# Optimization experiments

Measured on AMD Instinct MI355X. Metric: run time of the kernel, lower is better.

Reference implementation:

```python
import jax, jax.numpy as jnp
import numpy as np

B, S, D = 2, 2048, 1024
H, HD = 16, 64  # num_heads, head_dim; D == H*HD


def setup_inputs() -> dict:
    key = jax.random.key(0)
    k_x, k_wa, k_wp = jax.random.split(key, 3)
    x = jax.random.normal(k_x, (B, S, D), dtype=jnp.float32)
    w_attn = jax.random.normal(k_wa, (D, 3 * D), dtype=jnp.float32) * (1.0 / np.sqrt(D))
    b_attn = jnp.zeros((3 * D,), dtype=jnp.float32)
    w_proj = jax.random.normal(k_wp, (D, D), dtype=jnp.float32) * (1.0 / np.sqrt(D))
    b_proj = jnp.zeros((D,), dtype=jnp.float32)
    return {"x": x, "w_attn": w_attn, "b_attn": b_attn, "w_proj": w_proj, "b_proj": b_proj}


def reference(x, w_attn, b_attn, w_proj, b_proj):
    # c_attn: [B,S,D] -> [B,S,3D], split into q,k,v
    qkv = jnp.einsum('bsd,df->bsf', x, w_attn) + b_attn
    q, k, v = jnp.split(qkv, 3, axis=-1)
    # split heads: [B,S,D] -> [B,S,H,HD]
    q = q.reshape(B, S, H, HD)
    k = k.reshape(B, S, H, HD)
    v = v.reshape(B, S, H, HD)
    scale = 1.0 / jnp.sqrt(jnp.float32(HD))
    # scores: [B,H,S,S]
    scores = jnp.einsum('bnhd,bmhd->bhnm', q, k) * scale
    causal_mask = jnp.tril(jnp.ones((S, S), dtype=jnp.bool_))
    scores = jnp.where(causal_mask, scores, jnp.float32(-1e9))
    attn = jax.nn.softmax(scores, axis=-1)
    # dropout is identity (inference=True / p=0)
    out = jnp.einsum('bhnm,bmhd->bnhd', attn, v)
    out = out.reshape(B, S, D)
    out = jnp.einsum('bsd,de->bse', out, w_proj) + b_proj
    return out
```

## Files before the change

kernel.cpp:

```cpp
#include <hip/hip_runtime.h>

#define Bn 2
#define Sn 2048
#define Dn 1024
#define Hn 16
#define HDn 64

typedef unsigned short u16;
typedef u16 u16x4 __attribute__((ext_vector_type(4)));
typedef u16 u16x8 __attribute__((ext_vector_type(8)));
typedef __bf16 bf16x8 __attribute__((ext_vector_type(8)));
typedef float f32x4 __attribute__((ext_vector_type(4)));

__device__ __forceinline__ u16 cvt1(float f) {
  __bf16 h = (__bf16)f;
  return __builtin_bit_cast(u16, h);
}

__device__ __forceinline__ f32x4 mfma16(u16x8 a, u16x8 b, f32x4 c) {
  return __builtin_amdgcn_mfma_f32_16x16x32_bf16(
      __builtin_bit_cast(bf16x8, a), __builtin_bit_cast(bf16x8, b), c, 0, 0, 0);
}

__device__ __forceinline__ int xorv(int row) {
  return (row & 7) ^ ((row >> 3) & 7);
}
__device__ __forceinline__ int swzb(int row, int bytecol) {
  return row * 128 + (bytecol ^ (xorv(row) << 4));
}

__global__ __launch_bounds__(256) void k_cvt(const float* __restrict__ in,
                                             u16* __restrict__ out, int n4) {
  int i = blockIdx.x * 256 + threadIdx.x;
  if (i < n4) {
    const float4 v = reinterpret_cast<const float4*>(in)[i];
    u16x4 o = {cvt1(v.x), cvt1(v.y), cvt1(v.z), cvt1(v.w)};
    reinterpret_cast<u16x4*>(out)[i] = o;
  }
}

__global__ __launch_bounds__(256) void k_transpose(const float* __restrict__ in,
                                                   u16* __restrict__ out,
                                                   int K, int N) {
  __shared__ u16 tile[32][33];
  const int n0 = blockIdx.x * 32, k0 = blockIdx.y * 32;
  const int tx = threadIdx.x, ty = threadIdx.y;
#pragma unroll
  for (int r = 0; r < 4; ++r) {
    const int k = ty * 4 + r;
    tile[k][tx] = cvt1(in[(size_t)(k0 + k) * N + n0 + tx]);
  }
  __syncthreads();
#pragma unroll
  for (int r = 0; r < 4; ++r) {
    const int n = ty * 4 + r;
    out[(size_t)(n0 + n) * K + k0 + tx] = tile[tx][n];
  }
}

__global__ __launch_bounds__(512) void k_gemm2(
    const u16* __restrict__ A, const u16* __restrict__ Bt, int K,
    const float* __restrict__ bias, u16* __restrict__ oq, u16* __restrict__ ok,
    u16* __restrict__ ov, float* __restrict__ of, int mode) {
  __shared__ __align__(16) u16 a_lds[2][8192];
  __shared__ __align__(16) u16 b_lds[2][8192];
  const int tid = threadIdx.x;
  const int lane = tid & 63, w = tid >> 6;
  const int wr = w >> 2, wc = w & 3;
  const int lm = lane & 15, lk = lane >> 4;
  const int m0 = blockIdx.y * 128, n0 = blockIdx.x * 128;
  const int NT = K >> 6;

  const int srow0 = tid >> 3;
  const int scb = (tid & 7) * 16;

  f32x4 acc[4][2] = {};

#define STAGE2(d, kt)                                                         \
  {                                                                           \
    _Pragma("unroll") for (int p = 0; p < 2; ++p) {                           \
      const int row = p * 64 + srow0;                                         \
      const int col = (scb ^ (xorv(row) << 4)) >> 1;                          \
      __builtin_amdgcn_global_load_lds(                                       \
          (const __attribute__((address_space(1))) void*)(A + (size_t)(m0 + row) * K + (kt) * 64 + col), \
          (__attribute__((address_space(3))) void*)(a_lds[d] + p * 4096 + tid * 8), \
          16, 0, 0);                                                          \
      __builtin_amdgcn_global_load_lds(                                       \
          (const __attribute__((address_space(1))) void*)(Bt + (size_t)(n0 + row) * K + (kt) * 64 + col), \
          (__attribute__((address_space(3))) void*)(b_lds[d] + p * 4096 + tid * 8), \
          16, 0, 0);                                                          \
    }                                                                         \
  }

  STAGE2(0, 0);
  __syncthreads();

  for (int t = 0; t < NT; ++t) {
    const int cur = t & 1;
    if (t + 1 < NT) STAGE2(cur ^ 1, t + 1);
    u16x8 av[4][2], bv[2][2];
#pragma unroll
    for (int m = 0; m < 4; ++m)
#pragma unroll
      for (int kk = 0; kk < 2; ++kk)
        av[m][kk] = *reinterpret_cast<const u16x8*>(
            (char*)a_lds[cur] + swzb(wr * 64 + m * 16 + lm, kk * 64 + lk * 16));
#pragma unroll
    for (int n = 0; n < 2; ++n)
#pragma unroll
      for (int kk = 0; kk < 2; ++kk)
        bv[n][kk] = *reinterpret_cast<const u16x8*>(
            (char*)b_lds[cur] + swzb(wc * 32 + n * 16 + lm, kk * 64 + lk * 16));
    __builtin_amdgcn_s_setprio(1);
#pragma unroll
    for (int kk = 0; kk < 2; ++kk)
#pragma unroll
      for (int m = 0; m < 4; ++m)
#pragma unroll
        for (int n = 0; n < 2; ++n)
          acc[m][n] = mfma16(av[m][kk], bv[n][kk], acc[m][n]);
    __builtin_amdgcn_s_setprio(0);
    __syncthreads();
  }
#undef STAGE2

#pragma unroll
  for (int m = 0; m < 4; ++m) {
#pragma unroll
    for (int n = 0; n < 2; ++n) {
      const int col = n0 + wc * 32 + n * 16 + lm;
      const float bb = bias[col];
      const int row0 = m0 + wr * 64 + m * 16 + lk * 4;
      if (mode == 0) {
        const int which = col >> 10;
        const int h = (col >> 6) & 15, hd = col & 63;
        const int b = row0 >> 11, s0 = row0 & 2047;
        if (which == 2) {
          u16x4 pk;
#pragma unroll
          for (int j = 0; j < 4; ++j) pk[j] = cvt1(acc[m][n][j] + bb);
          *reinterpret_cast<u16x4*>(
              ov + ((size_t)(b * Hn + h) * HDn + hd) * Sn + s0) = pk;
        } else {
          u16* dst = which == 0 ? oq : ok;
          const float sc = which == 0 ? 0.125f : 1.0f;
#pragma unroll
          for (int j = 0; j < 4; ++j)
            dst[((size_t)(b * Hn + h) * Sn + s0 + j) * HDn + hd] =
                cvt1((acc[m][n][j] + bb) * sc);
        }
      } else {
#pragma unroll
        for (int j = 0; j < 4; ++j)
          of[(size_t)(row0 + j) * Dn + col] = acc[m][n][j] + bb;
      }
    }
  }
}

__global__ __launch_bounds__(256) void k_attn(const u16* __restrict__ qb,
                                              const u16* __restrict__ kb,
                                              const u16* __restrict__ vtb,
                                              u16* __restrict__ ob) {
  const int bx = blockIdx.x;
  const int qt = 31 - (bx >> 5);
  const int bh = bx & 31;
  const int h = bh & 15, b = bh >> 4;
  const int tid = threadIdx.x, lane = tid & 63, w = tid >> 6;
  const int lm = lane & 15, lk = lane >> 4;
  const int Q0 = qt * 64;
  const int q0 = Q0 + w * 16;
  const size_t head = (size_t)(b * Hn + h) * Sn * HDn;
  const u16* Q = qb + head;
  const u16* Kp = kb + head;
  const u16* Vt = vtb + head;

  __shared__ __align__(16) u16 k_lds[64 * 64];
  __shared__ __align__(16) u16 vt_lds[64 * 64];
  __shared__ __align__(16) u16 p_lds[4][16 * 64];
  char* myp = (char*)p_lds[w];

  const int sr = tid >> 2, scb = (tid & 3) * 16;
  const u16* Ksrc = Kp + (size_t)sr * HDn + scb;
  const u16* Vsrc = Vt + (size_t)sr * Sn + scb;

  u16x8 aq[2];
#pragma unroll
  for (int c = 0; c < 2; ++c)
    aq[c] = *reinterpret_cast<const u16x8*>(Q + (size_t)(q0 + lm) * HDn + c * 32 + lk * 8);

  f32x4 o_acc[4] = {};
  float mrow = -1e30f, lrow = 0.f;
  const float C = 1.44269504f;

  const int nk = Q0 + 64;
  u16x8 kreg[2], vreg[2];
  kreg[0] = *reinterpret_cast<const u16x8*>(Ksrc);
  kreg[1] = *reinterpret_cast<const u16x8*>(Ksrc + 8);
  vreg[0] = *reinterpret_cast<const u16x8*>(Vsrc);
  vreg[1] = *reinterpret_cast<const u16x8*>(Vsrc + 8);

  for (int j0 = 0; j0 < nk; j0 += 64) {
    *reinterpret_cast<u16x8*>((char*)k_lds + swzb(sr, scb * 2)) = kreg[0];
    *reinterpret_cast<u16x8*>((char*)k_lds + swzb(sr, scb * 2 + 16)) = kreg[1];
    *reinterpret_cast<u16x8*>((char*)vt_lds + swzb(sr, scb * 2)) = vreg[0];
    *reinterpret_cast<u16x8*>((char*)vt_lds + swzb(sr, scb * 2 + 16)) = vreg[1];
    __syncthreads();
    if (j0 + 64 < nk) {
      const u16* kn = Ksrc + (size_t)(j0 + 64) * HDn;
      const u16* vn = Vsrc + (j0 + 64);
      kreg[0] = *reinterpret_cast<const u16x8*>(kn);
      kreg[1] = *reinterpret_cast<const u16x8*>(kn + 8);
      vreg[0] = *reinterpret_cast<const u16x8*>(vn);
      vreg[1] = *reinterpret_cast<const u16x8*>(vn + 8);
    }

    f32x4 s[4];
    __builtin_amdgcn_s_setprio(1);
#pragma unroll
    for (int kc = 0; kc < 4; ++kc) {
      const u16x8 kf0 = *reinterpret_cast<const u16x8*>((char*)k_lds + swzb(kc * 16 + lm, lk * 16));
      const u16x8 kf1 = *reinterpret_cast<const u16x8*>((char*)k_lds + swzb(kc * 16 + lm, 64 + lk * 16));
      f32x4 z = {};
      z = mfma16(kf0, aq[0], z);
      s[kc] = mfma16(kf1, aq[1], z);
    }
    __builtin_amdgcn_s_setprio(0);
    if (j0 + 63 > q0) {
#pragma unroll
      for (int kc = 0; kc < 4; ++kc)
#pragma unroll
        for (int jj = 0; jj < 4; ++jj)
          if (j0 + kc * 16 + lk * 4 + jj > q0 + lm) s[kc][jj] = -1e30f;
    }

    float vmax = -1e30f;
#pragma unroll
    for (int kc = 0; kc < 4; ++kc)
#pragma unroll
      for (int jj = 0; jj < 4; ++jj) vmax = fmaxf(vmax, s[kc][jj]);
    vmax = fmaxf(vmax, __shfl_xor(vmax, 16, 64));
    vmax = fmaxf(vmax, __shfl_xor(vmax, 32, 64));
    if (!__all(vmax - mrow <= 8.0f)) {
      const float mnew = fmaxf(mrow, vmax);
      const float alpha = exp2f((mrow - mnew) * C);
      mrow = mnew;
      lrow *= alpha;
      float a4[4];
#pragma unroll
      for (int jj = 0; jj < 4; ++jj) a4[jj] = __shfl(alpha, lk * 4 + jj, 64);
#pragma unroll
      for (int t = 0; t < 4; ++t)
#pragma unroll
        for (int jj = 0; jj < 4; ++jj) o_acc[t][jj] *= a4[jj];
    }
    const float mc = mrow * C;
    float psum = 0.f;
#pragma unroll
    for (int kc = 0; kc < 4; ++kc) {
      u16x4 pk;
#pragma unroll
      for (int jj = 0; jj < 4; ++jj) {
        const float p = exp2f(s[kc][jj] * C - mc);
        psum += p;
        pk[jj] = cvt1(p);
      }
      *reinterpret_cast<u16x4*>(myp + swzb(lm, kc * 32 + lk * 8)) = pk;
    }
    psum += __shfl_xor(psum, 16, 64);
    psum += __shfl_xor(psum, 32, 64);
    lrow += psum;

    __builtin_amdgcn_s_setprio(1);
#pragma unroll
    for (int kt = 0; kt < 2; ++kt) {
      const u16x8 pa = *reinterpret_cast<const u16x8*>(myp + swzb(lm, kt * 64 + lk * 16));
#pragma unroll
      for (int t = 0; t < 4; ++t) {
        const u16x8 vf = *reinterpret_cast<const u16x8*>((char*)vt_lds + swzb(t * 16 + lm, kt * 64 + lk * 16));
        o_acc[t] = mfma16(pa, vf, o_acc[t]);
      }
    }
    __builtin_amdgcn_s_setprio(0);
    __syncthreads();
  }

  float l4[4];
#pragma unroll
  for (int jj = 0; jj < 4; ++jj) l4[jj] = __shfl(lrow, lk * 4 + jj, 64);
#pragma unroll
  for (int t = 0; t < 4; ++t) {
#pragma unroll
    for (int jj = 0; jj < 4; ++jj) {
      const int rowg = q0 + lk * 4 + jj;
      const float val = o_acc[t][jj] / l4[jj];
      ob[((size_t)(b * Sn + rowg)) * Dn + h * HDn + t * 16 + lm] = cvt1(val);
    }
  }
}

extern "C" void kernel_launch(void* const* d_in, const int* in_sizes, int n_in,
                              void* d_out, int out_size, void* d_ws, size_t ws_size,
                              hipStream_t stream) {
  const float* x = (const float*)d_in[0];
  const float* w_attn = (const float*)d_in[1];
  const float* b_attn = (const float*)d_in[2];
  const float* w_proj = (const float*)d_in[3];
  const float* b_proj = (const float*)d_in[4];
  float* out = (float*)d_out;

  u16* ws = (u16*)d_ws;
  u16* xb = ws;
  u16* wat = xb + (size_t)4096 * 1024;
  u16* wpt = wat + (size_t)3072 * 1024;
  u16* qb = wpt + (size_t)1024 * 1024;
  u16* kb = qb + (size_t)Bn * Hn * Sn * HDn;
  u16* vtb = kb + (size_t)Bn * Hn * Sn * HDn;
  u16* ao = vtb + (size_t)Bn * Hn * Sn * HDn;

  k_cvt<<<4096, 256, 0, stream>>>(x, xb, 1048576);
  k_transpose<<<dim3(3072 / 32, 1024 / 32), dim3(32, 8), 0, stream>>>(w_attn, wat, 1024, 3072);
  k_transpose<<<dim3(1024 / 32, 1024 / 32), dim3(32, 8), 0, stream>>>(w_proj, wpt, 1024, 1024);
  k_gemm2<<<dim3(3072 / 128, 4096 / 128), 512, 0, stream>>>(xb, wat, 1024, b_attn, qb, kb, vtb, nullptr, 0);
  k_attn<<<Bn * Hn * (Sn / 64), 256, 0, stream>>>(qb, kb, vtb, ao);
  k_gemm2<<<dim3(1024 / 128, 4096 / 128), 512, 0, stream>>>(ao, wpt, 1024, b_proj, nullptr, nullptr, nullptr, out, 1);
}
```

Baseline: 188.7 us.

## Double attention query tile per block with double-buffered K/V and XCD-aware GEMM block remap

The attention kernel now processes 128 query rows per block (32 per wave, two 16-row fragments), so each K/V tile loaded into LDS is reused across twice as many queries. K/V LDS staging is double-buffered, which lets the next tile be written while the current one is consumed. Fully masked fragments skip their MFMAs. The GEMM remaps linear block IDs across 8 groups, intended to improve L2 locality per XCD. In exchange, the attention grid has half as many blocks and needs more registers, which can lower occupancy.

```diff
diff --git a/kernel.cpp b/kernel.cpp
--- a/kernel.cpp
+++ b/kernel.cpp
@@ -68,7 +68,11 @@
   const int lane = tid & 63, w = tid >> 6;
   const int wr = w >> 2, wc = w & 3;
   const int lm = lane & 15, lk = lane >> 4;
-  const int m0 = blockIdx.y * 128, n0 = blockIdx.x * 128;
+  const int nx = gridDim.x;
+  int lin = blockIdx.y * nx + blockIdx.x;
+  const int cpx = (nx * gridDim.y) >> 3;
+  lin = (lin & 7) * cpx + (lin >> 3);
+  const int m0 = (lin / nx) * 128, n0 = (lin % nx) * 128;
   const int NT = K >> 6;
 
   const int srow0 = tid >> 3;
@@ -163,138 +167,182 @@
                                               const u16* __restrict__ vtb,
                                               u16* __restrict__ ob) {
   const int bx = blockIdx.x;
-  const int qt = 31 - (bx >> 5);
+  const int qt = 15 - (bx >> 5);
   const int bh = bx & 31;
   const int h = bh & 15, b = bh >> 4;
   const int tid = threadIdx.x, lane = tid & 63, w = tid >> 6;
   const int lm = lane & 15, lk = lane >> 4;
-  const int Q0 = qt * 64;
-  const int q0 = Q0 + w * 16;
+  const int Q0 = qt * 128;
+  const int q0 = Q0 + w * 32;
   const size_t head = (size_t)(b * Hn + h) * Sn * HDn;
   const u16* Q = qb + head;
   const u16* Kp = kb + head;
   const u16* Vt = vtb + head;
 
-  __shared__ __align__(16) u16 k_lds[64 * 64];
-  __shared__ __align__(16) u16 vt_lds[64 * 64];
-  __shared__ __align__(16) u16 p_lds[4][16 * 64];
+  __shared__ __align__(16) u16 k_lds[2][64 * 64];
+  __shared__ __align__(16) u16 vt_lds[2][64 * 64];
+  __shared__ __align__(16) u16 p_lds[4][32 * 64];
   char* myp = (char*)p_lds[w];
 
   const int sr = tid >> 2, scb = (tid & 3) * 16;
   const u16* Ksrc = Kp + (size_t)sr * HDn + scb;
   const u16* Vsrc = Vt + (size_t)sr * Sn + scb;
 
-  u16x8 aq[2];
-#pragma unroll
-  for (int c = 0; c < 2; ++c)
-    aq[c] = *reinterpret_cast<const u16x8*>(Q + (size_t)(q0 + lm) * HDn + c * 32 + lk * 8);
-
-  f32x4 o_acc[4] = {};
-  float mrow = -1e30f, lrow = 0.f;
+  u16x8 aq[2][2];
+#pragma unroll
+  for (int f = 0; f < 2; ++f)
+#pragma unroll
+    for (int c = 0; c < 2; ++c)
+      aq[f][c] = *reinterpret_cast<const u16x8*>(
+          Q + (size_t)(q0 + f * 16 + lm) * HDn + c * 32 + lk * 8);
+
+  f32x4 o_acc[2][4] = {};
+  float mrow[2] = {-1e30f, -1e30f}, lrow[2] = {0.f, 0.f};
   const float C = 1.44269504f;
 
-  const int nk = Q0 + 64;
+  const int NT = (Q0 + 128) >> 6;
   u16x8 kreg[2], vreg[2];
+
   kreg[0] = *reinterpret_cast<const u16x8*>(Ksrc);
   kreg[1] = *reinterpret_cast<const u16x8*>(Ksrc + 8);
   vreg[0] = *reinterpret_cast<const u16x8*>(Vsrc);
   vreg[1] = *reinterpret_cast<const u16x8*>(Vsrc + 8);
-
-  for (int j0 = 0; j0 < nk; j0 += 64) {
-    *reinterpret_cast<u16x8*>((char*)k_lds + swzb(sr, scb * 2)) = kreg[0];
-    *reinterpret_cast<u16x8*>((char*)k_lds + swzb(sr, scb * 2 + 16)) = kreg[1];
-    *reinterpret_cast<u16x8*>((char*)vt_lds + swzb(sr, scb * 2)) = vreg[0];
-    *reinterpret_cast<u16x8*>((char*)vt_lds + swzb(sr, scb * 2 + 16)) = vreg[1];
-    __syncthreads();
-    if (j0 + 64 < nk) {
-      const u16* kn = Ksrc + (size_t)(j0 + 64) * HDn;
-      const u16* vn = Vsrc + (j0 + 64);
-      kreg[0] = *reinterpret_cast<const u16x8*>(kn);
-      kreg[1] = *reinterpret_cast<const u16x8*>(kn + 8);
-      vreg[0] = *reinterpret_cast<const u16x8*>(vn);
-      vreg[1] = *reinterpret_cast<const u16x8*>(vn + 8);
-    }
-
-    f32x4 s[4];
+  *reinterpret_cast<u16x8*>((char*)k_lds[0] + swzb(sr, scb * 2)) = kreg[0];
+  *reinterpret_cast<u16x8*>((char*)k_lds[0] + swzb(sr, scb * 2 + 16)) = kreg[1];
+  *reinterpret_cast<u16x8*>((char*)vt_lds[0] + swzb(sr, scb * 2)) = vreg[0];
+  *reinterpret_cast<u16x8*>((char*)vt_lds[0] + swzb(sr, scb * 2 + 16)) = vreg[1];
+  {
+    const u16* kn = Ksrc + (size_t)64 * HDn;
+    const u16* vn = Vsrc + 64;
+    kreg[0] = *reinterpret_cast<const u16x8*>(kn);
+    kreg[1] = *reinterpret_cast<const u16x8*>(kn + 8);
+    vreg[0] = *reinterpret_cast<const u16x8*>(vn);
+    vreg[1] = *reinterpret_cast<const u16x8*>(vn + 8);
+  }
+  __syncthreads();
+
+  for (int t = 0; t < NT; ++t) {
+    const int cur = t & 1;
+    const int j0 = t * 64;
+    if (t + 1 < NT) {
+      *reinterpret_cast<u16x8*>((char*)k_lds[cur ^ 1] + swzb(sr, scb * 2)) = kreg[0];
+      *reinterpret_cast<u16x8*>((char*)k_lds[cur ^ 1] + swzb(sr, scb * 2 + 16)) = kreg[1];
+      *reinterpret_cast<u16x8*>((char*)vt_lds[cur ^ 1] + swzb(sr, scb * 2)) = vreg[0];
+      *reinterpret_cast<u16x8*>((char*)vt_lds[cur ^ 1] + swzb(sr, scb * 2 + 16)) = vreg[1];
+      if (t + 2 < NT) {
+        const u16* kn = Ksrc + (size_t)(j0 + 128) * HDn;
+        const u16* vn = Vsrc + (j0 + 128);
+        kreg[0] = *reinterpret_cast<const u16x8*>(kn);
+        kreg[1] = *reinterpret_cast<const u16x8*>(kn + 8);
+        vreg[0] = *reinterpret_cast<const u16x8*>(vn);
+        vreg[1] = *reinterpret_cast<const u16x8*>(vn + 8);
+      }
+    }
+
+    const bool act[2] = {j0 <= q0 + 15, j0 <= q0 + 31};
+
+    f32x4 s[2][4];
     __builtin_amdgcn_s_setprio(1);
 #pragma unroll
     for (int kc = 0; kc < 4; ++kc) {
-      const u16x8 kf0 = *reinterpret_cast<const u16x8*>((char*)k_lds + swzb(kc * 16 + lm, lk * 16));
-      const u16x8 kf1 = *reinterpret_cast<const u16x8*>((char*)k_lds + swzb(kc * 16 + lm, 64 + lk * 16));
-      f32x4 z = {};
-      z = mfma16(kf0, aq[0], z);
-      s[kc] = mfma16(kf1, aq[1], z);
+      const u16x8 kf0 = *reinterpret_cast<const u16x8*>(
+          (char*)k_lds[cur] + swzb(kc * 16 + lm, lk * 16));
+      const u16x8 kf1 = *reinterpret_cast<const u16x8*>(
+          (char*)k_lds[cur] + swzb(kc * 16 + lm, 64 + lk * 16));
+#pragma unroll
+      for (int f = 0; f < 2; ++f) {
+        if (!act[f]) continue;
+        f32x4 z = {};
+        z = mfma16(kf0, aq[f][0], z);
+        s[f][kc] = mfma16(kf1, aq[f][1], z);
+      }
     }
     __builtin_amdgcn_s_setprio(0);
-    if (j0 + 63 > q0) {
+
+#pragma unroll
+    for (int f = 0; f < 2; ++f) {
+      if (!act[f]) continue;
+      const int q0f = q0 + f * 16;
+      if (j0 + 63 > q0f) {
+#pragma unroll
+        for (int kc = 0; kc < 4; ++kc)
+#pragma unroll
+          for (int jj = 0; jj < 4; ++jj)
+            if (j0 + kc * 16 + lk * 4 + jj > q0f + lm) s[f][kc][jj] = -1e30f;
+      }
+      float vmax = -1e30f;
 #pragma unroll
       for (int kc = 0; kc < 4; ++kc)
 #pragma unroll
-        for (int jj = 0; jj < 4; ++jj)
-          if (j0 + kc * 16 + lk * 4 + jj > q0 + lm) s[kc][jj] = -1e30f;
-    }
-
-    float vmax = -1e30f;
-#pragma unroll
-    for (int kc = 0; kc < 4; ++kc)
-#pragma unroll
-      for (int jj = 0; jj < 4; ++jj) vmax = fmaxf(vmax, s[kc][jj]);
-    vmax = fmaxf(vmax, __shfl_xor(vmax, 16, 64));
-    vmax = fmaxf(vmax, __shfl_xor(vmax, 32, 64));
-    if (!__all(vmax - mrow <= 8.0f)) {
-      const float mnew = fmaxf(mrow, vmax);
-      const float alpha = exp2f((mrow - mnew) * C);
-      mrow = mnew;
-      lrow *= alpha;
-      float a4[4];
-#pragma unroll
-      for (int jj = 0; jj < 4; ++jj) a4[jj] = __shfl(alpha, lk * 4 + jj, 64);
-#pragma unroll
-      for (int t = 0; t < 4; ++t)
-#pragma unroll
-        for (int jj = 0; jj < 4; ++jj) o_acc[t][jj] *= a4[jj];
-    }
-    const float mc = mrow * C;
-    float psum = 0.f;
-#pragma unroll
-    for (int kc = 0; kc < 4; ++kc) {
-      u16x4 pk;
-#pragma unroll
-      for (int jj = 0; jj < 4; ++jj) {
-        const float p = exp2f(s[kc][jj] * C - mc);
-        psum += p;
-        pk[jj] = cvt1(p);
-      }
-      *reinterpret_cast<u16x4*>(myp + swzb(lm, kc * 32 + lk * 8)) = pk;
-    }
-    psum += __shfl_xor(psum, 16, 64);
-    psum += __shfl_xor(psum, 32, 64);
-    lrow += psum;
+        for (int jj = 0; jj < 4; ++jj) vmax = fmaxf(vmax, s[f][kc][jj]);
+      vmax = fmaxf(vmax, __shfl_xor(vmax, 16, 64));
+      vmax = fmaxf(vmax, __shfl_xor(vmax, 32, 64));
+      if (!__all(vmax - mrow[f] <= 8.0f)) {
+        const float mnew = fmaxf(mrow[f], vmax);
+        const float alpha = exp2f((mrow[f] - mnew) * C);
+        mrow[f] = mnew;
+        lrow[f] *= alpha;
+        float a4[4];
+#pragma unroll
+        for (int jj = 0; jj < 4; ++jj) a4[jj] = __shfl(alpha, lk * 4 + jj, 64);
+#pragma unroll
+        for (int tt = 0; tt < 4; ++tt)
+#pragma unroll
+          for (int jj = 0; jj < 4; ++jj) o_acc[f][tt][jj] *= a4[jj];
+      }
+      const float mc = mrow[f] * C;
+      float psum = 0.f;
+#pragma unroll
+      for (int kc = 0; kc < 4; ++kc) {
+        u16x4 pk;
+#pragma unroll
+        for (int jj = 0; jj < 4; ++jj) {
+          const float p = exp2f(s[f][kc][jj] * C - mc);
+          psum += p;
+          pk[jj] = cvt1(p);
+        }
+        *reinterpret_cast<u16x4*>(myp + swzb(f * 16 + lm, kc * 32 + lk * 8)) = pk;
+      }
+      psum += __shfl_xor(psum, 16, 64);
+      psum += __shfl_xor(psum, 32, 64);
+      lrow[f] += psum;
+    }
 
     __builtin_amdgcn_s_setprio(1);
 #pragma unroll
     for (int kt = 0; kt < 2; ++kt) {
-      const u16x8 pa = *reinterpret_cast<const u16x8*>(myp + swzb(lm, kt * 64 + lk * 16));
-#pragma unroll
-      for (int t = 0; t < 4; ++t) {
-        const u16x8 vf = *reinterpret_cast<const u16x8*>((char*)vt_lds + swzb(t * 16 + lm, kt * 64 + lk * 16));
-        o_acc[t] = mfma16(pa, vf, o_acc[t]);
+      u16x8 vf[4];
+#pragma unroll
+      for (int tt = 0; tt < 4; ++tt)
+        vf[tt] = *reinterpret_cast<const u16x8*>(
+            (char*)vt_lds[cur] + swzb(tt * 16 + lm, kt * 64 + lk * 16));
+#pragma unroll
+      for (int f = 0; f < 2; ++f) {
+        if (!act[f]) continue;
+        const u16x8 pa = *reinterpret_cast<const u16x8*>(
+            myp + swzb(f * 16 + lm, kt * 64 + lk * 16));
+#pragma unroll
+        for (int tt = 0; tt < 4; ++tt)
+          o_acc[f][tt] = mfma16(pa, vf[tt], o_acc[f][tt]);
       }
     }
     __builtin_amdgcn_s_setprio(0);
     __syncthreads();
   }
 
-  float l4[4];
-#pragma unroll
-  for (int jj = 0; jj < 4; ++jj) l4[jj] = __shfl(lrow, lk * 4 + jj, 64);
-#pragma unroll
-  for (int t = 0; t < 4; ++t) {
-#pragma unroll
-    for (int jj = 0; jj < 4; ++jj) {
-      const int rowg = q0 + lk * 4 + jj;
-      const float val = o_acc[t][jj] / l4[jj];
-      ob[((size_t)(b * Sn + rowg)) * Dn + h * HDn + t * 16 + lm] = cvt1(val);
+#pragma unroll
+  for (int f = 0; f < 2; ++f) {
+    float l4[4];
+#pragma unroll
+    for (int jj = 0; jj < 4; ++jj) l4[jj] = __shfl(lrow[f], lk * 4 + jj, 64);
+#pragma unroll
+    for (int tt = 0; tt < 4; ++tt) {
+#pragma unroll
+      for (int jj = 0; jj < 4; ++jj) {
+        const int rowg = q0 + f * 16 + lk * 4 + jj;
+        const float val = o_acc[f][tt][jj] / l4[jj];
+        ob[((size_t)(b * Sn + rowg)) * Dn + h * HDn + tt * 16 + lm] = cvt1(val);
+      }
     }
   }
 }
@@ -322,6 +370,6 @@
   k_transpose<<<dim3(3072 / 32, 1024 / 32), dim3(32, 8), 0, stream>>>(w_attn, wat, 1024, 3072);
   k_transpose<<<dim3(1024 / 32, 1024 / 32), dim3(32, 8), 0, stream>>>(w_proj, wpt, 1024, 1024);
   k_gemm2<<<dim3(3072 / 128, 4096 / 128), 512, 0, stream>>>(xb, wat, 1024, b_attn, qb, kb, vtb, nullptr, 0);
-  k_attn<<<Bn * Hn * (Sn / 64), 256, 0, stream>>>(qb, kb, vtb, ao);
+  k_attn<<<Bn * Hn * (Sn / 128), 256, 0, stream>>>(qb, kb, vtb, ao);
   k_gemm2<<<dim3(1024 / 128, 4096 / 128), 512, 0, stream>>>(ao, wpt, 1024, b_proj, nullptr, nullptr, nullptr, out, 1);
 }
```

Result: slower. 206.9 us (+9.6%).
